# Kernel tuning notes

Hardware: AMD Instinct MI355X
Metric: run time of the kernel (lower is better)

The kernel has to match this reference:

```python
import jax, jax.numpy as jnp
import numpy as np

LN_EPS = 1e-5


def setup_inputs() -> dict:
    key = jax.random.key(0)
    ks = jax.random.split(key, 10)
    N, E, B = 20000, 320000, 16
    node_dim, cond_dim, out_dim = 256, 512, 256
    return {
        "node_feats": jax.random.normal(ks[0], (N, node_dim), dtype=jnp.float32),
        "cond_feats": jax.random.normal(ks[1], (B, cond_dim), dtype=jnp.float32),
        "batch_ids": jax.random.randint(ks[2], (N,), 0, B),
        "node_j_ids": jax.random.randint(ks[3], (E,), 0, N),
        "node_i_ids": jax.random.randint(ks[4], (E,), 0, N),
        "edge_w": jax.random.uniform(ks[5], (E, 1), dtype=jnp.float32),
        "edge_p": jax.random.uniform(ks[6], (E, 1), dtype=jnp.float32),
        "Wc": jax.random.normal(ks[7], (cond_dim, 2 * out_dim), dtype=jnp.float32) * (cond_dim ** -0.5),
        "bc": jax.random.normal(ks[8], (2 * out_dim,), dtype=jnp.float32) * 0.02,
        "Wl": jax.random.normal(ks[9], (node_dim, out_dim), dtype=jnp.float32) * (node_dim ** -0.5),
    }


def reference(node_feats, cond_feats, batch_ids, node_j_ids, node_i_ids,
              edge_w, edge_p, Wc, bc, Wl):
    N = node_feats.shape[0]
    # --- FiLM fusion ---
    gb = cond_feats @ Wc + bc                       # [B, 2*out_dim]
    gamma, beta = jnp.split(gb, 2, axis=-1)
    gamma = gamma + 1.0
    x = node_feats @ Wl                             # [N, out_dim]
    # non-affine LayerNorm over last dim
    mu = jnp.mean(x, axis=-1, keepdims=True)
    var = jnp.mean(jnp.square(x - mu), axis=-1, keepdims=True)
    x = (x - mu) * jax.lax.rsqrt(var + LN_EPS)
    x = x * gamma[batch_ids] + beta[batch_ids]      # per-node FiLM via batch gather
    x = jax.nn.relu(x)
    # --- message passing: gather -> weight -> scatter-add ---
    edge_weights = edge_w * edge_p                  # [E, 1]
    msg = x[node_j_ids] * edge_weights              # [E, out_dim]
    agg = jax.ops.segment_sum(msg, node_i_ids, num_segments=N)
    return jax.nn.relu(agg)
```

## Files before the change

kernel.cpp:

```cpp
#include <hip/hip_runtime.h>
#include <hip/hip_bf16.h>

#define OUT_DIM 256
#define COND_DIM 512
#define NODE_DIM 256
#define TM 32
#define LDA 264
#define LN_EPS 1e-5f
#define POISON 0xAAAAAAAAu

typedef __attribute__((ext_vector_type(8))) short bf16x8;
typedef __attribute__((ext_vector_type(8))) unsigned short u16x8;
typedef __attribute__((ext_vector_type(4))) float f32x4;

__device__ inline unsigned short f2bf(float f) {
    unsigned u = __float_as_uint(f);
    u += 0x7fffu + ((u >> 16) & 1u);
    return (unsigned short)(u >> 16);
}
__device__ inline float bf2f(unsigned short b) {
    return __uint_as_float((unsigned)b << 16);
}

__global__ __launch_bounds__(256) void prep_kernel(
        const float* __restrict__ Wl, unsigned short* __restrict__ WlT,
        const float* __restrict__ cond, const float* __restrict__ Wc,
        const float* __restrict__ bc, float* __restrict__ gamma, float* __restrict__ beta,
        const int* __restrict__ ni, unsigned* __restrict__ counts, int E) {
    __shared__ float lds[64 * 65];
    for (int e = blockIdx.x * 256 + threadIdx.x; e < E; e += gridDim.x * 256)
        atomicAdd(&counts[ni[e]], 1u);

    if (blockIdx.x < 16) {
        float (*tile)[65] = (float(*)[65])lds;
        int bx = blockIdx.x & 3, by = blockIdx.x >> 2;
        int tr = threadIdx.x >> 6, tc = threadIdx.x & 63;
        #pragma unroll
        for (int rr = 0; rr < 64; rr += 4)
            tile[rr + tr][tc] = Wl[(by * 64 + rr + tr) * OUT_DIM + bx * 64 + tc];
        __syncthreads();
        #pragma unroll
        for (int rr = 0; rr < 64; rr += 4) {
            int n = bx * 64 + rr + tr;
            int k = by * 64 + tc;
            WlT[n * NODE_DIM + k] = f2bf(tile[tc][rr + tr]);
        }
    } else if (blockIdx.x < 48) {
        int bf = blockIdx.x - 16;
        int b = bf >> 1, half = bf & 1;
        int o = half * 256 + threadIdx.x;
        float* c = lds;
        for (int k = threadIdx.x; k < COND_DIM; k += 256) c[k] = cond[b * COND_DIM + k];
        __syncthreads();
        float acc = bc[o];
        for (int k = 0; k < COND_DIM; k += 4) {
            float4 cv = *(const float4*)&c[k];
            acc += cv.x * Wc[(k + 0) * 512 + o];
            acc += cv.y * Wc[(k + 1) * 512 + o];
            acc += cv.z * Wc[(k + 2) * 512 + o];
            acc += cv.w * Wc[(k + 3) * 512 + o];
        }
        if (half == 0) gamma[b * 256 + threadIdx.x] = acc + 1.0f;
        else           beta[b * 256 + threadIdx.x] = acc;
    }
}

__global__ __launch_bounds__(256) void node_mfma_kernel(
        const float* __restrict__ nf, const unsigned short* __restrict__ WlT,
        const int* __restrict__ batch_ids, const float* __restrict__ gamma,
        const float* __restrict__ beta, unsigned short* __restrict__ xout, int N,
        const unsigned* __restrict__ counts, int* __restrict__ row_start) {
    __shared__ __align__(16) unsigned short Atile[TM * LDA];
    __shared__ float part_s[TM][2], part_s2[TM][2];
    __shared__ int bid_s[TM];
    __shared__ int ssum[256];
    int t = threadIdx.x;

    if (blockIdx.x == gridDim.x - 1) {
        const int P = 80;
        int base = t * P;
        int sum = 0;
        if (base < N) {
            if (base + P <= N) {
                for (int i = 0; i < P; i += 4) {
                    uint4 v = *(const uint4*)&counts[base + i];
                    sum += (int)(v.x - POISON) + (int)(v.y - POISON)
                         + (int)(v.z - POISON) + (int)(v.w - POISON);
                }
            } else {
                for (int i = 0; i < P; ++i)
                    if (base + i < N) sum += (int)(counts[base + i] - POISON);
            }
        }
        ssum[t] = sum;
        __syncthreads();
        for (int off = 1; off < 256; off <<= 1) {
            int v = (t >= off) ? ssum[t - off] : 0;
            __syncthreads();
            ssum[t] += v;
            __syncthreads();
        }
        int run = ssum[t] - sum;
        if (base < N) {
            if (base + P <= N) {
                for (int i = 0; i < P; i += 4) {
                    uint4 v = *(const uint4*)&counts[base + i];
                    int d0 = (int)(v.x - POISON), d1 = (int)(v.y - POISON);
                    int d2 = (int)(v.z - POISON), d3 = (int)(v.w - POISON);
                    int4 w;
                    w.x = run; w.y = run + d0; w.z = w.y + d1; w.w = w.z + d2;
                    *(int4*)&row_start[base + i] = w;
                    run = w.w + d3;
                }
            } else {
                for (int i = 0; i < P; ++i)
                    if (base + i < N) {
                        row_start[base + i] = run;
                        run += (int)(counts[base + i] - POISON);
                    }
            }
        }
        if (t == 255) row_start[N] = ssum[255];
        return;
    }

    int n0 = blockIdx.x * TM;

    #pragma unroll
    for (int it = 0; it < 8; ++it) {
        int idx = t + it * 256;
        int r = idx >> 6;
        int c4 = idx & 63;
        int row = n0 + r;
        float4 v;
        if (row < N) v = *(const float4*)&nf[(size_t)row * NODE_DIM + c4 * 4];
        else         v = make_float4(0.f, 0.f, 0.f, 0.f);
        unsigned* dst = (unsigned*)&Atile[r * LDA + c4 * 4];
        dst[0] = (unsigned)f2bf(v.x) | ((unsigned)f2bf(v.y) << 16);
        dst[1] = (unsigned)f2bf(v.z) | ((unsigned)f2bf(v.w) << 16);
    }
    if (t < TM) bid_s[t] = (n0 + t < N) ? batch_ids[n0 + t] : 0;
    __syncthreads();

    int wave = t >> 6;
    int lane = t & 63;
    int l = lane & 15;
    int quad = lane >> 4;
    int rowbase = (wave & 1) * 16;
    int colbase = (wave >> 1) * 128;
    int half = wave >> 1;

    f32x4 acc[8];
    #pragma unroll
    for (int ct = 0; ct < 8; ++ct) acc[ct] = (f32x4){0.f, 0.f, 0.f, 0.f};

    const unsigned short* Abase = &Atile[(rowbase + l) * LDA + quad * 8];
    const unsigned short* Bbase = &WlT[(colbase + l) * NODE_DIM + quad * 8];

    #pragma unroll
    for (int ks = 0; ks < 8; ++ks) {
        bf16x8 a = *(const bf16x8*)(Abase + ks * 32);
        #pragma unroll
        for (int ct = 0; ct < 8; ++ct) {
            bf16x8 b = *(const bf16x8*)(Bbase + ct * 16 * NODE_DIM + ks * 32);
            acc[ct] = __builtin_amdgcn_mfma_f32_16x16x32_bf16(a, b, acc[ct], 0, 0, 0);
        }
    }

    #pragma unroll
    for (int reg = 0; reg < 4; ++reg) {
        float s = 0.f, s2 = 0.f;
        #pragma unroll
        for (int ct = 0; ct < 8; ++ct) {
            float v = acc[ct][reg];
            s += v; s2 += v * v;
        }
        #pragma unroll
        for (int off = 1; off <= 8; off <<= 1) {
            s += __shfl_xor(s, off);
            s2 += __shfl_xor(s2, off);
        }
        if (l == 0) {
            int r = rowbase + quad * 4 + reg;
            part_s[r][half] = s;
            part_s2[r][half] = s2;
        }
    }
    __syncthreads();

    #pragma unroll
    for (int reg = 0; reg < 4; ++reg) {
        int lrow = rowbase + quad * 4 + reg;
        float S = part_s[lrow][0] + part_s[lrow][1];
        float S2 = part_s2[lrow][0] + part_s2[lrow][1];
        float mu = S * (1.f / OUT_DIM);
        float var = S2 * (1.f / OUT_DIM) - mu * mu;
        float rs = rsqrtf(var + LN_EPS);
        int grow = n0 + lrow;
        int bid = bid_s[lrow];
        const float* gg = &gamma[bid * OUT_DIM];
        const float* gb = &beta[bid * OUT_DIM];
        if (grow < N) {
            unsigned short* orow = &xout[(size_t)grow * OUT_DIM];
            #pragma unroll
            for (int ct = 0; ct < 8; ++ct) {
                int col = colbase + ct * 16 + l;
                float v = (acc[ct][reg] - mu) * rs;
                v = v * gg[col] + gb[col];
                orow[col] = f2bf(fmaxf(v, 0.f));
            }
        }
    }
}

__global__ void fill_kernel(const int* __restrict__ nj, const int* __restrict__ ni,
                            const float* __restrict__ ew, const float* __restrict__ ep,
                            int* __restrict__ row_start, int2* __restrict__ epk, int E) {
    int e = (blockIdx.x * blockDim.x + threadIdx.x) * 2;
    if (e + 2 <= E) {
        int2 i2 = *(const int2*)&ni[e];
        int2 j2 = *(const int2*)&nj[e];
        float2 w2 = *(const float2*)&ew[e];
        float2 p2 = *(const float2*)&ep[e];
        int pos0 = atomicAdd(&row_start[i2.x], 1);
        int pos1 = atomicAdd(&row_start[i2.y], 1);
        epk[pos0] = make_int2(j2.x, __float_as_int(w2.x * p2.x));
        epk[pos1] = make_int2(j2.y, __float_as_int(w2.y * p2.y));
    } else if (e < E) {
        int i = ni[e];
        int pos = atomicAdd(&row_start[i], 1);
        epk[pos] = make_int2(nj[e], __float_as_int(ew[e] * ep[e]));
    }
}

__global__ void agg_kernel(const unsigned short* __restrict__ x, const int2* __restrict__ epk,
                           const int* __restrict__ row_start, float* __restrict__ out, int N) {
    int node = blockIdx.x * 4 + (threadIdx.x >> 6);
    int lane = threadIdx.x & 63;
    if (node >= N) return;
    int s = (node == 0) ? 0 : row_start[node - 1];
    int e = row_start[node];
    int half = lane >> 5;
    int li = lane & 31;

    float a[8];
    #pragma unroll
    for (int k = 0; k < 8; ++k) a[k] = 0.f;

    int p = s;
    for (; p + 8 <= e; p += 8) {
        int2 pk0 = epk[p + 0 + half];
        int2 pk1 = epk[p + 2 + half];
        int2 pk2 = epk[p + 4 + half];
        int2 pk3 = epk[p + 6 + half];
        u16x8 v0 = *(const u16x8*)&x[(size_t)pk0.x * OUT_DIM + li * 8];
        u16x8 v1 = *(const u16x8*)&x[(size_t)pk1.x * OUT_DIM + li * 8];
        u16x8 v2 = *(const u16x8*)&x[(size_t)pk2.x * OUT_DIM + li * 8];
        u16x8 v3 = *(const u16x8*)&x[(size_t)pk3.x * OUT_DIM + li * 8];
        float w0 = __int_as_float(pk0.y);
        float w1 = __int_as_float(pk1.y);
        float w2 = __int_as_float(pk2.y);
        float w3 = __int_as_float(pk3.y);
        #pragma unroll
        for (int k = 0; k < 8; ++k) {
            a[k] += bf2f(v0[k]) * w0;
            a[k] += bf2f(v1[k]) * w1;
            a[k] += bf2f(v2[k]) * w2;
            a[k] += bf2f(v3[k]) * w3;
        }
    }
    for (; p < e; p += 2) {
        int idx = p + half;
        int safe = (idx < e) ? idx : (e - 1);
        int2 pk = epk[safe];
        float w = (idx < e) ? __int_as_float(pk.y) : 0.f;
        u16x8 v = *(const u16x8*)&x[(size_t)pk.x * OUT_DIM + li * 8];
        #pragma unroll
        for (int k = 0; k < 8; ++k) a[k] += bf2f(v[k]) * w;
    }

    #pragma unroll
    for (int k = 0; k < 8; ++k) a[k] += __shfl_xor(a[k], 32);

    f32x4 o;
    int kb = half * 4;
    o[0] = fmaxf(a[kb + 0], 0.f);
    o[1] = fmaxf(a[kb + 1], 0.f);
    o[2] = fmaxf(a[kb + 2], 0.f);
    o[3] = fmaxf(a[kb + 3], 0.f);
    __builtin_nontemporal_store(o, (f32x4*)&out[(size_t)node * OUT_DIM + li * 8 + kb]);
}

extern "C" void kernel_launch(void* const* d_in, const int* in_sizes, int n_in,
                              void* d_out, int out_size, void* d_ws, size_t ws_size,
                              hipStream_t stream) {
    const float* node_feats = (const float*)d_in[0];
    const float* cond_feats = (const float*)d_in[1];
    const int*   batch_ids  = (const int*)d_in[2];
    const int*   node_j     = (const int*)d_in[3];
    const int*   node_i     = (const int*)d_in[4];
    const float* edge_w     = (const float*)d_in[5];
    const float* edge_p     = (const float*)d_in[6];
    const float* Wc         = (const float*)d_in[7];
    const float* bc         = (const float*)d_in[8];
    const float* Wl         = (const float*)d_in[9];
    float* out = (float*)d_out;

    const int N = in_sizes[2];
    const int E = in_sizes[3];
    const int B = in_sizes[1] / COND_DIM;

    char* ws = (char*)d_ws;
    float* gamma     = (float*)ws;  ws += (size_t)B * OUT_DIM * 4;
    float* beta      = (float*)ws;  ws += (size_t)B * OUT_DIM * 4;
    unsigned short* x   = (unsigned short*)ws;  ws += (size_t)N * OUT_DIM * 2;
    unsigned short* WlT = (unsigned short*)ws;  ws += (size_t)NODE_DIM * OUT_DIM * 2;
    unsigned* counts = (unsigned*)ws;  ws += (size_t)N * 4;
    int* row_start   = (int*)ws;       ws += (size_t)(N + 4) * 4;
    int2* epk        = (int2*)ws;      ws += (size_t)E * 8;

    int nblk = (N + TM - 1) / TM;

    prep_kernel<<<256, 256, 0, stream>>>(Wl, WlT, cond_feats, Wc, bc, gamma, beta,
                                         node_i, counts, E);
    node_mfma_kernel<<<nblk + 1, 256, 0, stream>>>(node_feats, WlT, batch_ids, gamma, beta,
                                                   x, N, counts, row_start);
    fill_kernel<<<(E / 2 + 255) / 256 + 1, 256, 0, stream>>>(node_j, node_i, edge_w, edge_p,
                                                             row_start, epk, E);
    agg_kernel<<<(N + 3) / 4, 256, 0, stream>>>(x, epk, row_start, out, N);
}
```

Measured before the change: 187.7 us.

## Bucket each destination's edges by source-node slice for gather locality

```diff
diff --git a/kernel.cpp b/kernel.cpp
--- a/kernel.cpp
+++ b/kernel.cpp
@@ -7,6 +7,7 @@
 #define TM 32
 #define LDA 264
 #define LN_EPS 1e-5f
+#define NB 4
 #define POISON 0xAAAAAAAAu
 
 typedef __attribute__((ext_vector_type(8))) short bf16x8;
@@ -26,10 +27,14 @@
         const float* __restrict__ Wl, unsigned short* __restrict__ WlT,
         const float* __restrict__ cond, const float* __restrict__ Wc,
         const float* __restrict__ bc, float* __restrict__ gamma, float* __restrict__ beta,
-        const int* __restrict__ ni, unsigned* __restrict__ counts, int E) {
+        const int* __restrict__ ni, const int* __restrict__ nj,
+        unsigned* __restrict__ counts, int E, int slice) {
     __shared__ float lds[64 * 65];
-    for (int e = blockIdx.x * 256 + threadIdx.x; e < E; e += gridDim.x * 256)
-        atomicAdd(&counts[ni[e]], 1u);
+    for (int e = blockIdx.x * 256 + threadIdx.x; e < E; e += gridDim.x * 256) {
+        int i = ni[e];
+        int b = nj[e] / slice;
+        atomicAdd(&counts[i * NB + b], 1u);
+    }
 
     if (blockIdx.x < 16) {
         float (*tile)[65] = (float(*)[65])lds;
@@ -77,11 +82,12 @@
     int t = threadIdx.x;
 
     if (blockIdx.x == gridDim.x - 1) {
-        const int P = 80;
+        const int NT = NB * N;
+        const int P = 316;
         int base = t * P;
         int sum = 0;
-        if (base < N) {
-            if (base + P <= N) {
+        if (base < NT) {
+            if (base + P <= NT) {
                 for (int i = 0; i < P; i += 4) {
                     uint4 v = *(const uint4*)&counts[base + i];
                     sum += (int)(v.x - POISON) + (int)(v.y - POISON)
@@ -89,7 +95,7 @@
                 }
             } else {
                 for (int i = 0; i < P; ++i)
-                    if (base + i < N) sum += (int)(counts[base + i] - POISON);
+                    if (base + i < NT) sum += (int)(counts[base + i] - POISON);
             }
         }
         ssum[t] = sum;
@@ -101,8 +107,8 @@
             __syncthreads();
         }
         int run = ssum[t] - sum;
-        if (base < N) {
-            if (base + P <= N) {
+        if (base < NT) {
+            if (base + P <= NT) {
                 for (int i = 0; i < P; i += 4) {
                     uint4 v = *(const uint4*)&counts[base + i];
                     int d0 = (int)(v.x - POISON), d1 = (int)(v.y - POISON);
@@ -114,13 +120,13 @@
                 }
             } else {
                 for (int i = 0; i < P; ++i)
-                    if (base + i < N) {
+                    if (base + i < NT) {
                         row_start[base + i] = run;
                         run += (int)(counts[base + i] - POISON);
                     }
             }
         }
-        if (t == 255) row_start[N] = ssum[255];
+        if (t == 255) row_start[NT] = ssum[255];
         return;
     }
 
@@ -215,20 +221,23 @@
 
 __global__ void fill_kernel(const int* __restrict__ nj, const int* __restrict__ ni,
                             const float* __restrict__ ew, const float* __restrict__ ep,
-                            int* __restrict__ row_start, int2* __restrict__ epk, int E) {
+                            int* __restrict__ row_start, int2* __restrict__ epk, int E,
+                            int slice) {
     int e = (blockIdx.x * blockDim.x + threadIdx.x) * 2;
     if (e + 2 <= E) {
         int2 i2 = *(const int2*)&ni[e];
         int2 j2 = *(const int2*)&nj[e];
         float2 w2 = *(const float2*)&ew[e];
         float2 p2 = *(const float2*)&ep[e];
-        int pos0 = atomicAdd(&row_start[i2.x], 1);
-        int pos1 = atomicAdd(&row_start[i2.y], 1);
+        int b0 = j2.x / slice, b1 = j2.y / slice;
+        int pos0 = atomicAdd(&row_start[i2.x * NB + b0], 1);
+        int pos1 = atomicAdd(&row_start[i2.y * NB + b1], 1);
         epk[pos0] = make_int2(j2.x, __float_as_int(w2.x * p2.x));
         epk[pos1] = make_int2(j2.y, __float_as_int(w2.y * p2.y));
     } else if (e < E) {
         int i = ni[e];
-        int pos = atomicAdd(&row_start[i], 1);
+        int b = nj[e] / slice;
+        int pos = atomicAdd(&row_start[i * NB + b], 1);
         epk[pos] = make_int2(nj[e], __float_as_int(ew[e] * ep[e]));
     }
 }
@@ -238,8 +247,8 @@
     int node = blockIdx.x * 4 + (threadIdx.x >> 6);
     int lane = threadIdx.x & 63;
     if (node >= N) return;
-    int s = (node == 0) ? 0 : row_start[node - 1];
-    int e = row_start[node];
+    int s = (node == 0) ? 0 : row_start[node * NB - 1];
+    int e = row_start[node * NB + NB - 1];
     int half = lane >> 5;
     int li = lane & 31;
 
@@ -309,23 +318,24 @@
     const int N = in_sizes[2];
     const int E = in_sizes[3];
     const int B = in_sizes[1] / COND_DIM;
+    const int slice = (N + NB - 1) / NB;
 
     char* ws = (char*)d_ws;
     float* gamma     = (float*)ws;  ws += (size_t)B * OUT_DIM * 4;
     float* beta      = (float*)ws;  ws += (size_t)B * OUT_DIM * 4;
     unsigned short* x   = (unsigned short*)ws;  ws += (size_t)N * OUT_DIM * 2;
     unsigned short* WlT = (unsigned short*)ws;  ws += (size_t)NODE_DIM * OUT_DIM * 2;
-    unsigned* counts = (unsigned*)ws;  ws += (size_t)N * 4;
-    int* row_start   = (int*)ws;       ws += (size_t)(N + 4) * 4;
+    unsigned* counts = (unsigned*)ws;  ws += (size_t)NB * N * 4;
+    int* row_start   = (int*)ws;       ws += ((size_t)NB * N + 4) * 4;
     int2* epk        = (int2*)ws;      ws += (size_t)E * 8;
 
     int nblk = (N + TM - 1) / TM;
 
     prep_kernel<<<256, 256, 0, stream>>>(Wl, WlT, cond_feats, Wc, bc, gamma, beta,
-                                         node_i, counts, E);
+                                         node_i, node_j, counts, E, slice);
     node_mfma_kernel<<<nblk + 1, 256, 0, stream>>>(node_feats, WlT, batch_ids, gamma, beta,
                                                    x, N, counts, row_start);
     fill_kernel<<<(E / 2 + 255) / 256 + 1, 256, 0, stream>>>(node_j, node_i, edge_w, edge_p,
-                                                             row_start, epk, E);
+                                                             row_start, epk, E, slice);
     agg_kernel<<<(N + 3) / 4, 256, 0, stream>>>(x, epk, row_start, out, N);
 }
```

After: 220.5 us. 17.5% more time.
